# Optimization experiments

Measured on AMD Instinct MI355X. Metric: run time of the kernel, lower is better.

## Reference

```python
import jax, jax.numpy as jnp
import numpy as np

E, T, D, H = 4, 4096, 2048, 8192

def setup_inputs() -> dict:
    key = jax.random.key(0)
    k1, k2, k3 = jax.random.split(key, 3)
    x = jax.random.normal(k1, (E, T, D), dtype=jnp.float32)
    fc1_w = jax.random.normal(k2, (E, D, H), dtype=jnp.float32) * 0.001
    fc2_w = jax.random.normal(k3, (E, H, D), dtype=jnp.float32) * 0.001
    fc1_b = jnp.zeros((E, 1, H), dtype=jnp.float32)
    fc2_b = jnp.zeros((E, 1, D), dtype=jnp.float32)
    return {"x": x, "fc1_w": fc1_w, "fc1_b": fc1_b, "fc2_w": fc2_w, "fc2_b": fc2_b}

def reference(x, fc1_w, fc1_b, fc2_w, fc2_b):
    # batched expert FFN: y = relu(x @ W1 + b1) @ W2 + b2, per expert e
    y = jnp.einsum('etd,edh->eth', x, fc1_w) + fc1_b
    y = jax.nn.relu(y)
    y = jnp.einsum('eth,ehd->etd', y, fc2_w) + fc2_b
    return y
```

## Files before the change

### kernel.cpp

```cpp
#include <hip/hip_runtime.h>
#include <hip/hip_bf16.h>
#include <stdint.h>

#define E_ 4
#define T_ 4096
#define D_ 2048
#define H_ 8192

typedef __attribute__((ext_vector_type(8))) short bf16x8;
typedef __attribute__((ext_vector_type(4))) float f32x4;

__device__ __forceinline__ unsigned short f2bf(float f) {
    unsigned int u = __float_as_uint(f);
    u = u + 0x7fffu + ((u >> 16) & 1u);
    return (unsigned short)(u >> 16);
}

__device__ __forceinline__ void async16(const unsigned short* g, unsigned short* l) {
    auto gp = (const __attribute__((address_space(1))) unsigned int*)g;
    auto lp = (__attribute__((address_space(3))) unsigned int*)l;
    __builtin_amdgcn_global_load_lds(gp, lp, 16 , 0 , 0 );
}

__device__ __forceinline__ f32x4 mfma16(bf16x8 a, bf16x8 b, f32x4 c) {
    return __builtin_amdgcn_mfma_f32_16x16x32_bf16(a, b, c, 0, 0, 0);
}

__global__ void cvt_x_kernel(const float4* __restrict__ in, uint2* __restrict__ out, long n4) {
    long i = (long)blockIdx.x * blockDim.x + threadIdx.x;
    long stride = (long)gridDim.x * blockDim.x;
    for (; i < n4; i += stride) {
        float4 v = in[i];
        uint2 o;
        o.x = (unsigned)f2bf(v.x) | ((unsigned)f2bf(v.y) << 16);
        o.y = (unsigned)f2bf(v.z) | ((unsigned)f2bf(v.w) << 16);
        out[i] = o;
    }
}

__global__ void transpose_cvt_kernel(const float* __restrict__ W, unsigned short* __restrict__ Wt,
                                     int R, int C) {
    __shared__ float tile[64][65];
    const float* Wp = W + (size_t)blockIdx.z * R * C;
    unsigned short* Wtp = Wt + (size_t)blockIdx.z * R * C;
    const int c0 = blockIdx.x * 64, r0 = blockIdx.y * 64;
    const int tc = threadIdx.x & 63;
    const int tr = threadIdx.x >> 6;
#pragma unroll
    for (int i = 0; i < 16; ++i) {
        int r = tr * 16 + i;
        tile[r][tc] = Wp[(size_t)(r0 + r) * C + c0 + tc];
    }
    __syncthreads();
#pragma unroll
    for (int i = 0; i < 16; ++i) {
        int r = tr * 16 + i;
        Wtp[(size_t)(c0 + r) * R + r0 + tc] = f2bf(tile[tc][r]);
    }
}

template <int K, int OUT_MODE>
__global__ __launch_bounds__(512, 2) void gemm256_kernel(
    const unsigned short* __restrict__ A,
    const unsigned short* __restrict__ Bt,
    const float* __restrict__ bias,
    void* __restrict__ Cout,
    int M, int N)
{
    constexpr int BK = 64;
    constexpr int NT = K / BK;
    __shared__ __align__(16) unsigned short L[2][2][2][128][64];

    const int nx = gridDim.x, ny = gridDim.y;
    const int nwg = nx * ny * gridDim.z;
    const int w = (blockIdx.z * ny + blockIdx.y) * nx + blockIdx.x;
    const int cpx = nwg >> 3;
    const int lid = (w & 7) * cpx + (w >> 3);
    const int e  = lid / (nx * ny);
    const int r2 = lid % (nx * ny);
    const int by = r2 / nx, bx = r2 % nx;

    const unsigned short* Ae = A + (size_t)e * M * K;
    const unsigned short* Be = Bt + (size_t)e * N * K;
    const int bm0 = by * 256;
    const int bn0 = bx * 256;

    const int tid = threadIdx.x;
    const int lane = tid & 63;
    const int wid = tid >> 6;
    const int wr = wid >> 2;
    const int wc = wid & 3;

    const int srow = wid * 16 + (lane >> 3);
    const int skel = 8 * ((lane & 7) ^ (lane >> 3));

    const int fr = lane & 15;
    const int kq = lane >> 4;
    const int ksw = (lane & 7) << 3;
    const int bh = wc >> 1;
    const int brb = (wc & 1) * 64;

    f32x4 acc[8][4] = {};

    auto stageA = [&](int t, int h) {
        const int k0 = t * BK;
        const int s = t & 1;
#pragma unroll
        for (int i = 0; i < 2; ++i) {
            async16(Ae + (size_t)(bm0 + h * 128 + srow + i * 8) * K + k0 + skel,
                    &L[s][0][h][wid * 16 + i * 8][0]);
        }
    };
    auto stageB = [&](int t, int h) {
        const int k0 = t * BK;
        const int s = t & 1;
#pragma unroll
        for (int i = 0; i < 2; ++i) {
            async16(Be + (size_t)(bn0 + h * 128 + srow + i * 8) * K + k0 + skel,
                    &L[s][1][h][wid * 16 + i * 8][0]);
        }
    };

    stageB(0, 0); stageB(0, 1); stageA(0, 0); stageA(0, 1);
    stageB(1, 0); stageB(1, 1); stageA(1, 0); stageA(1, 1);
    asm volatile("s_waitcnt vmcnt(8)" ::: "memory");
    __builtin_amdgcn_s_barrier();

    bf16x8 a[4][2], b[4][2];

    for (int t = 0; t < NT; ++t) {
        const int s = t & 1;

#pragma unroll
        for (int n = 0; n < 4; ++n)
#pragma unroll
            for (int kk = 0; kk < 2; ++kk)
                b[n][kk] = *(const bf16x8*)&L[s][1][bh][brb + n * 16 + fr][(kk * 32 + kq * 8) ^ ksw];
#pragma unroll
        for (int m = 0; m < 4; ++m)
#pragma unroll
            for (int kk = 0; kk < 2; ++kk)
                a[m][kk] = *(const bf16x8*)&L[s][0][wr][m * 16 + fr][(kk * 32 + kq * 8) ^ ksw];
        __builtin_amdgcn_s_barrier();
        __builtin_amdgcn_s_setprio(1);
#pragma unroll
        for (int m = 0; m < 4; ++m)
#pragma unroll
            for (int n = 0; n < 2; ++n)
#pragma unroll
                for (int kk = 0; kk < 2; ++kk)
                    acc[m][n] = mfma16(a[m][kk], b[n][kk], acc[m][n]);
        __builtin_amdgcn_s_setprio(0);
        asm volatile("s_waitcnt lgkmcnt(0)" ::: "memory");
        __builtin_amdgcn_s_barrier();

        if (t + 2 < NT) stageB(t + 2, 0);
        __builtin_amdgcn_s_barrier();
        __builtin_amdgcn_s_setprio(1);
#pragma unroll
        for (int m = 0; m < 4; ++m)
#pragma unroll
            for (int n = 2; n < 4; ++n)
#pragma unroll
                for (int kk = 0; kk < 2; ++kk)
                    acc[m][n] = mfma16(a[m][kk], b[n][kk], acc[m][n]);
        __builtin_amdgcn_s_setprio(0);
        __builtin_amdgcn_s_barrier();

#pragma unroll
        for (int m = 0; m < 4; ++m)
#pragma unroll
            for (int kk = 0; kk < 2; ++kk)
                a[m][kk] = *(const bf16x8*)&L[s][0][wr][(m + 4) * 16 + fr][(kk * 32 + kq * 8) ^ ksw];
        if (t + 2 < NT) stageB(t + 2, 1);
        __builtin_amdgcn_s_barrier();
        __builtin_amdgcn_s_setprio(1);
#pragma unroll
        for (int m = 0; m < 4; ++m)
#pragma unroll
            for (int n = 0; n < 2; ++n)
#pragma unroll
                for (int kk = 0; kk < 2; ++kk)
                    acc[m + 4][n] = mfma16(a[m][kk], b[n][kk], acc[m + 4][n]);
        __builtin_amdgcn_s_setprio(0);
        asm volatile("s_waitcnt lgkmcnt(0)" ::: "memory");
        __builtin_amdgcn_s_barrier();

        if (t + 2 < NT) {
            stageA(t + 2, 0); stageA(t + 2, 1);
            asm volatile("s_waitcnt vmcnt(8)" ::: "memory");
        } else {
            asm volatile("s_waitcnt vmcnt(0)" ::: "memory");
        }
        __builtin_amdgcn_s_barrier();
        __builtin_amdgcn_s_setprio(1);
#pragma unroll
        for (int m = 0; m < 4; ++m)
#pragma unroll
            for (int n = 2; n < 4; ++n)
#pragma unroll
                for (int kk = 0; kk < 2; ++kk)
                    acc[m + 4][n] = mfma16(a[m][kk], b[n][kk], acc[m + 4][n]);
        __builtin_amdgcn_s_setprio(0);
        __builtin_amdgcn_s_barrier();
    }

    const int rowq = (lane >> 4) * 4;
    const float* bp = bias + (size_t)e * N;

    if (OUT_MODE == 0) {
        unsigned short* Y = (unsigned short*)Cout + (size_t)e * M * N;
#pragma unroll
        for (int n = 0; n < 4; ++n) {
            const int cg = bn0 + wc * 64 + n * 16 + fr;
            const float bb = bp[cg];
#pragma unroll
            for (int m = 0; m < 8; ++m) {
                const int rg0 = bm0 + wr * 128 + m * 16 + rowq;
#pragma unroll
                for (int j = 0; j < 4; ++j) {
                    float v = acc[m][n][j] + bb;
                    v = fmaxf(v, 0.0f);
                    Y[(size_t)(rg0 + j) * N + cg] = f2bf(v);
                }
            }
        }
    } else {
        float* O = (float*)Cout + (size_t)e * M * N;
#pragma unroll
        for (int n = 0; n < 4; ++n) {
            const int cg = bn0 + wc * 64 + n * 16 + fr;
            const float bb = bp[cg];
#pragma unroll
            for (int m = 0; m < 8; ++m) {
                const int rg0 = bm0 + wr * 128 + m * 16 + rowq;
#pragma unroll
                for (int j = 0; j < 4; ++j) {
                    O[(size_t)(rg0 + j) * N + cg] = acc[m][n][j] + bb;
                }
            }
        }
    }
}

extern "C" void kernel_launch(void* const* d_in, const int* in_sizes, int n_in,
                              void* d_out, int out_size, void* d_ws, size_t ws_size,
                              hipStream_t stream) {
    const float* x     = (const float*)d_in[0];
    const float* fc1_w = (const float*)d_in[1];
    const float* fc1_b = (const float*)d_in[2];
    const float* fc2_w = (const float*)d_in[3];
    const float* fc2_b = (const float*)d_in[4];
    float* out = (float*)d_out;

    const size_t n_x  = (size_t)E_ * T_ * D_;
    const size_t n_w1 = (size_t)E_ * D_ * H_;
    const size_t n_w2 = (size_t)E_ * H_ * D_;
    const size_t n_y1 = (size_t)E_ * T_ * H_;

    const size_t need = (n_x + n_w1 + n_w2 + n_y1) * sizeof(unsigned short);
    if (ws_size < need) return;

    unsigned short* xb  = (unsigned short*)d_ws;
    unsigned short* w1t = xb + n_x;
    unsigned short* w2t = w1t + n_w1;
    unsigned short* y1  = w2t + n_w2;

    cvt_x_kernel<<<2048, 256, 0, stream>>>((const float4*)x, (uint2*)xb, (long)(n_x / 4));
    {
        dim3 g(H_ / 64, D_ / 64, E_);
        transpose_cvt_kernel<<<g, 256, 0, stream>>>(fc1_w, w1t, D_, H_);
    }
    {
        dim3 g(D_ / 64, H_ / 64, E_);
        transpose_cvt_kernel<<<g, 256, 0, stream>>>(fc2_w, w2t, H_, D_);
    }
    {
        dim3 g(H_ / 256, T_ / 256, E_);
        gemm256_kernel<D_, 0><<<g, 512, 0, stream>>>(xb, w1t, fc1_b, (void*)y1, T_, H_);
    }
    {
        dim3 g(D_ / 256, T_ / 256, E_);
        gemm256_kernel<H_, 1><<<g, 512, 0, stream>>>(y1, w2t, fc2_b, (void*)out, T_, D_);
    }
}
```

Before: 1.224 ms.

## Restructure GEMM main loop into two MFMA phases with fewer barriers

Reorganizes the double-buffered K loop from four MFMA quarter-phases with eight barriers into two half-phases with two barriers per iteration. All B fragments and the first A half are read from LDS up front, and the second A half is read during the first MFMA block. All next-stage global-to-LDS loads are issued together after the LDS reads complete. The vmcnt wait moves to the top of each iteration, which reduces synchronization overhead but makes global loads arrive in a burst instead of being interleaved with compute.

```diff
diff --git a/kernel.cpp b/kernel.cpp
--- a/kernel.cpp
+++ b/kernel.cpp
@@ -123,16 +123,21 @@
 
     stageB(0, 0); stageB(0, 1); stageA(0, 0); stageA(0, 1);
     stageB(1, 0); stageB(1, 1); stageA(1, 0); stageA(1, 1);
-    asm volatile("s_waitcnt vmcnt(8)" ::: "memory");
-    __builtin_amdgcn_s_barrier();
 
     bf16x8 a[4][2], b[4][2];
 
     for (int t = 0; t < NT; ++t) {
         const int s = t & 1;
 
-#pragma unroll
-        for (int n = 0; n < 4; ++n)
+        if (t == NT - 1) {
+            asm volatile("s_waitcnt vmcnt(0)" ::: "memory");
+        } else {
+            asm volatile("s_waitcnt vmcnt(8)" ::: "memory");
+        }
+        __builtin_amdgcn_s_barrier();
+
+#pragma unroll
+        for (int n = 0; n < 2; ++n)
 #pragma unroll
             for (int kk = 0; kk < 2; ++kk)
                 b[n][kk] = *(const bf16x8*)&L[s][1][bh][brb + n * 16 + fr][(kk * 32 + kq * 8) ^ ksw];
@@ -141,68 +146,46 @@
 #pragma unroll
             for (int kk = 0; kk < 2; ++kk)
                 a[m][kk] = *(const bf16x8*)&L[s][0][wr][m * 16 + fr][(kk * 32 + kq * 8) ^ ksw];
-        __builtin_amdgcn_s_barrier();
+#pragma unroll
+        for (int n = 2; n < 4; ++n)
+#pragma unroll
+            for (int kk = 0; kk < 2; ++kk)
+                b[n][kk] = *(const bf16x8*)&L[s][1][bh][brb + n * 16 + fr][(kk * 32 + kq * 8) ^ ksw];
+
         __builtin_amdgcn_s_setprio(1);
 #pragma unroll
         for (int m = 0; m < 4; ++m)
 #pragma unroll
-            for (int n = 0; n < 2; ++n)
+            for (int n = 0; n < 4; ++n)
 #pragma unroll
                 for (int kk = 0; kk < 2; ++kk)
                     acc[m][n] = mfma16(a[m][kk], b[n][kk], acc[m][n]);
         __builtin_amdgcn_s_setprio(0);
+
+#pragma unroll
+        for (int m = 0; m < 4; ++m)
+#pragma unroll
+            for (int kk = 0; kk < 2; ++kk)
+                a[m][kk] = *(const bf16x8*)&L[s][0][wr][(m + 4) * 16 + fr][(kk * 32 + kq * 8) ^ ksw];
+
         asm volatile("s_waitcnt lgkmcnt(0)" ::: "memory");
         __builtin_amdgcn_s_barrier();
 
-        if (t + 2 < NT) stageB(t + 2, 0);
-        __builtin_amdgcn_s_barrier();
+        if (t + 2 < NT) {
+            stageB(t + 2, 0); stageB(t + 2, 1);
+            stageA(t + 2, 0); stageA(t + 2, 1);
+        }
+        __builtin_amdgcn_sched_barrier(0);
+
         __builtin_amdgcn_s_setprio(1);
 #pragma unroll
         for (int m = 0; m < 4; ++m)
 #pragma unroll
-            for (int n = 2; n < 4; ++n)
-#pragma unroll
-                for (int kk = 0; kk < 2; ++kk)
-                    acc[m][n] = mfma16(a[m][kk], b[n][kk], acc[m][n]);
-        __builtin_amdgcn_s_setprio(0);
-        __builtin_amdgcn_s_barrier();
-
-#pragma unroll
-        for (int m = 0; m < 4; ++m)
-#pragma unroll
-            for (int kk = 0; kk < 2; ++kk)
-                a[m][kk] = *(const bf16x8*)&L[s][0][wr][(m + 4) * 16 + fr][(kk * 32 + kq * 8) ^ ksw];
-        if (t + 2 < NT) stageB(t + 2, 1);
-        __builtin_amdgcn_s_barrier();
-        __builtin_amdgcn_s_setprio(1);
-#pragma unroll
-        for (int m = 0; m < 4; ++m)
-#pragma unroll
-            for (int n = 0; n < 2; ++n)
+            for (int n = 0; n < 4; ++n)
 #pragma unroll
                 for (int kk = 0; kk < 2; ++kk)
                     acc[m + 4][n] = mfma16(a[m][kk], b[n][kk], acc[m + 4][n]);
         __builtin_amdgcn_s_setprio(0);
-        asm volatile("s_waitcnt lgkmcnt(0)" ::: "memory");
-        __builtin_amdgcn_s_barrier();
-
-        if (t + 2 < NT) {
-            stageA(t + 2, 0); stageA(t + 2, 1);
-            asm volatile("s_waitcnt vmcnt(8)" ::: "memory");
-        } else {
-            asm volatile("s_waitcnt vmcnt(0)" ::: "memory");
-        }
-        __builtin_amdgcn_s_barrier();
-        __builtin_amdgcn_s_setprio(1);
-#pragma unroll
-        for (int m = 0; m < 4; ++m)
-#pragma unroll
-            for (int n = 2; n < 4; ++n)
-#pragma unroll
-                for (int kk = 0; kk < 2; ++kk)
-                    acc[m + 4][n] = mfma16(a[m][kk], b[n][kk], acc[m + 4][n]);
-        __builtin_amdgcn_s_setprio(0);
-        __builtin_amdgcn_s_barrier();
     }
 
     const int rowq = (lane >> 4) * 4;
```

Result: no change. 1.210 ms (-1.2%).
